# Kernel tuning notes

Hardware: AMD Instinct MI355X
Metric: run time of the kernel (lower is better)

Reference implementation:

```python
import jax, jax.numpy as jnp
from jax import lax
import numpy as np

# Config mirroring init_kwargs
B, N, PD = 4, 16384, 3
PROJ = 64                 # projection_channel
M1, K1, C1 = 2048, 32, 128  # level-1 SA: fps points, neighbors, out channel
M2, K2, C2 = 512, 32, 256   # level-2 SA
DH, DO = 512, 256           # dense hidden / out (dense_channels)


def fps(pts, M):
    """Farthest point sampling. pts: [N,3] -> indices [M] (starts at point 0)."""
    n = pts.shape[0]
    def step(carry, _):
        dmin, last = carry
        d = jnp.sum((pts - pts[last]) ** 2, axis=-1)   # dist to newest center
        dmin = jnp.minimum(dmin, d)
        nxt = jnp.argmax(dmin).astype(jnp.int32)
        return (dmin, nxt), last
    init = (jnp.full((n,), 1e10, pts.dtype), jnp.int32(0))
    _, idxs = lax.scan(step, init, None, length=M)
    return idxs


def sa_level(pts, feats, M, K, Wa, ba, Wb, bb):
    """PointNet++ set abstraction: FPS + kNN (xyz space) + grouped MLP + max."""
    idx = jax.vmap(lambda p: fps(p, M))(pts)                       # [B,M]
    centers = jnp.take_along_axis(pts, idx[:, :, None], axis=1)    # [B,M,3]
    d = jnp.sum((centers[:, :, None, :] - pts[:, None, :, :]) ** 2, -1)  # [B,M,N]
    _, nidx = lax.top_k(-d, K)                                      # [B,M,K]
    gather = jax.vmap(lambda a, i: a[i])
    rel = gather(pts, nidx) - centers[:, :, None, :]                # [B,M,K,3]
    nf = gather(feats, nidx)                                        # [B,M,K,C]
    g = jnp.concatenate([rel, nf], axis=-1)                         # use_xyz=True
    h = jax.nn.relu(g @ Wa + ba)
    h = jax.nn.relu(h @ Wb + bb)
    return centers, jnp.max(h, axis=2)                              # [B,M,Cout]


def setup_inputs() -> dict:
    key = jax.random.key(0)
    ks = jax.random.split(key, 12)
    w = lambda k, shape, s: jax.random.normal(k, shape, jnp.float32) * s
    z = lambda c: jnp.zeros((c,), jnp.float32)
    return {
        "xyz": jax.random.normal(ks[0], (B, N, PD), jnp.float32),
        "Wp": w(ks[1], (PD, PROJ), 0.3), "bp": z(PROJ),
        "W1a": w(ks[2], (PROJ + 3, C1), 0.1), "b1a": z(C1),
        "W1b": w(ks[3], (C1, C1), 0.08), "b1b": z(C1),
        "W2a": w(ks[4], (C1 + 3, C2), 0.08), "b2a": z(C2),
        "W2b": w(ks[5], (C2, C2), 0.06), "b2b": z(C2),
        "Wd1": w(ks[6], (2 * C2, DH), 0.05), "bd1": z(DH),
        "Wd2": w(ks[7], (DH, DO), 0.05), "bd2": z(DO),
    }


def reference(xyz, Wp, bp, W1a, b1a, W1b, b1b, W2a, b2a, W2b, b2b,
              Wd1, bd1, Wd2, bd2):
    feats = xyz @ Wp + bp            # point_proj: [B,N,PROJ]
    pts = xyz[..., :3]
    pts, feats = sa_level(pts, feats, M1, K1, W1a, b1a, W1b, b1b)
    pts, feats = sa_level(pts, feats, M2, K2, W2a, b2a, W2b, b2b)
    # global max + avg pool (adaptive_max/avg_pool1d to 1), concat -> [B,2*C2]
    g = jnp.concatenate([jnp.max(feats, axis=1), jnp.mean(feats, axis=1)], -1)
    h = jax.nn.relu(g @ Wd1 + bd1)   # DenseBlock w/ activation
    return h @ Wd2 + bd2             # last block: no activation (last_activation=False)
```

## Files before the change

kernel.cpp:

```cpp
#include <hip/hip_runtime.h>

#define B_    4
#define N1_   16384
#define M1_   2048
#define M2_   512
#define KNN_  32
#define PROJ_ 64
#define C1_   128
#define C2_   256
#define PROJ_BLKS_ ((B_ * N1_ * PROJ_) / 512)
#define KNN_BLKS_  ((M1_ / 64) * (B_ * 64))

__device__ __forceinline__ float sqdist_exact(float px, float py, float pz,
                                              float cx, float cy, float cz) {
    float dx = __fsub_rn(px, cx);
    float dy = __fsub_rn(py, cy);
    float dz = __fsub_rn(pz, cz);
    return __fadd_rn(__fadd_rn(__fmul_rn(dx, dx), __fmul_rn(dy, dy)), __fmul_rn(dz, dz));
}

typedef float v2f __attribute__((ext_vector_type(2)));

template<int CTRL, int RM>
__device__ __forceinline__ unsigned long long dpp_umax64(unsigned long long pk) {
    unsigned lo = (unsigned)__builtin_amdgcn_update_dpp(
        0, (int)(unsigned)pk, CTRL, RM, 0xf, true);
    unsigned hi = (unsigned)__builtin_amdgcn_update_dpp(
        0, (int)(unsigned)(pk >> 32), CTRL, RM, 0xf, true);
    unsigned long long o = ((unsigned long long)hi << 32) | (unsigned long long)lo;
    return (o > pk) ? o : pk;
}

__device__ __forceinline__ unsigned long long wave_max_key(unsigned long long pk) {
    pk = dpp_umax64<0x111, 0xf>(pk);
    pk = dpp_umax64<0x112, 0xf>(pk);
    pk = dpp_umax64<0x114, 0xf>(pk);
    pk = dpp_umax64<0x118, 0xf>(pk);
    pk = dpp_umax64<0x142, 0xa>(pk);
    pk = dpp_umax64<0x143, 0xc>(pk);
    return pk;
}

__device__ __forceinline__ unsigned reduce8_widx(const unsigned long long* wk,
                                                 int lane) {
    unsigned long long k8 = wk[lane & 7];
    k8 = dpp_umax64<0x111, 0xf>(k8);
    k8 = dpp_umax64<0x112, 0xf>(k8);
    k8 = dpp_umax64<0x114, 0xf>(k8);
    unsigned lo = (unsigned)__builtin_amdgcn_readlane((int)(unsigned)k8, 7);
    return ~lo;
}

__device__ __forceinline__ unsigned reduce2_widx(const unsigned long long* wk,
                                                 int lane) {
    unsigned long long k2 = wk[lane & 1];
    k2 = dpp_umax64<0x111, 0xf>(k2);
    unsigned lo = (unsigned)__builtin_amdgcn_readlane((int)(unsigned)k2, 1);
    return ~lo;
}

template<int N>
__device__ void knn_body512(const float* __restrict__ P,
                            float cx, float cy, float cz,
                            int* __restrict__ out, char* arena) {
    constexpr int K = KNN_;
    constexpr int CAP = 224;
    const int t = threadIdx.x;
    const int lane = t & 63;
    const int w = t >> 6;

    int*      hist = (int*)arena;
    unsigned* eqk  = (unsigned*)(arena + 8192);
    int*      eqi  = (int*)(arena + 8192 + 896);
    int*      wsum = (int*)(arena + 8192 + 1792);
    int*      ctrl = (int*)(arena + 8192 + 1824);

    unsigned prefix = 0; int pbits = 0;
    unsigned Tlo = 0; unsigned long long Thi = 0x100000000ull;
    int L = 0, target = K, Cbin = N;

    for (int round = 0; round < 3; ++round) {
        const int bits  = (round < 2) ? 11 : 10;
        const int nbins = 1 << bits;
        const int shift = 32 - pbits - bits;
        for (int i = t; i < nbins; i += 512) hist[i] = 0;
        __syncthreads();
        for (int j = t; j < N; j += 512) {
            float d = sqdist_exact(P[j * 3], P[j * 3 + 1], P[j * 3 + 2], cx, cy, cz);
            unsigned key = __float_as_uint(d);
            if (key >= Tlo && (unsigned long long)key < Thi)
                atomicAdd(&hist[(key >> shift) & (nbins - 1)], 1);
        }
        __syncthreads();
        const int per = nbins / 512;
        int s = 0;
        for (int i = 0; i < per; ++i) s += hist[t * per + i];
        int cum = s;
        for (int off = 1; off < 64; off <<= 1) {
            int o = __shfl_up(cum, off);
            if (lane >= off) cum += o;
        }
        if (lane == 63) wsum[w] = cum;
        __syncthreads();
        int wpre = 0;
        for (int i = 0; i < w; ++i) wpre += wsum[i];
        cum += wpre;
        const int cumex = cum - s;
        if ((cumex < target) && (cum >= target)) {
            int acc = cumex;
            for (int i = 0; i < per; ++i) {
                int h = hist[t * per + i];
                if (acc + h >= target) { ctrl[2] = t * per + i; ctrl[3] = acc; ctrl[4] = h; break; }
                acc += h;
            }
        }
        __syncthreads();
        const int binsel = ctrl[2];
        const int Ladd   = ctrl[3];
        const int bincnt = ctrl[4];
        L += Ladd;
        target -= Ladd;
        prefix = (prefix << bits) | (unsigned)binsel;
        pbits += bits;
        Tlo = prefix << (32 - pbits);
        Thi = ((unsigned long long)prefix + 1ull) << (32 - pbits);
        Cbin = bincnt;
        __syncthreads();
        if (Cbin <= CAP) break;
    }

    if (t == 0) { ctrl[0] = 0; ctrl[1] = 0; }
    __syncthreads();

    if (Cbin <= CAP) {
        for (int j = t; j < N; j += 512) {
            float d = sqdist_exact(P[j * 3], P[j * 3 + 1], P[j * 3 + 2], cx, cy, cz);
            unsigned key = __float_as_uint(d);
            if (key < Tlo) {
                int p = atomicAdd(&ctrl[0], 1);
                out[p] = j;
            } else if ((unsigned long long)key < Thi) {
                int p = atomicAdd(&ctrl[1], 1);
                eqk[p] = key; eqi[p] = j;
            }
        }
        __syncthreads();
        const int E = ctrl[1];
        for (int e = t; e < E; e += 512) {
            unsigned ke = eqk[e]; int ie = eqi[e];
            int rank = 0;
            for (int f = 0; f < E; ++f) {
                unsigned kf = eqk[f]; int jf = eqi[f];
                rank += (kf < ke || (kf == ke && jf < ie)) ? 1 : 0;
            }
            if (rank < target) out[L + rank] = ie;
        }
    } else {
        if (t < 64) {
            int cnt = 0;
            for (int jb = 0; jb < N; jb += 64) {
                int j = jb + lane;
                float d = sqdist_exact(P[j * 3], P[j * 3 + 1], P[j * 3 + 2], cx, cy, cz);
                unsigned key = __float_as_uint(d);
                if (key < Tlo) {
                    int p = atomicAdd(&ctrl[0], 1);
                    out[p] = j;
                }
                bool eq = (key == Tlo);
                unsigned long long mb = __ballot(eq);
                int below = __popcll(mb & ((1ull << lane) - 1ull));
                if (eq && (cnt + below) < target) out[L + cnt + below] = j;
                cnt += (int)__popcll(mb);
            }
        }
    }
}

__global__ __attribute__((amdgpu_flat_work_group_size(512, 512)))
__attribute__((amdgpu_waves_per_eu(2, 2)))
void mega1_kernel(const float* __restrict__ xyz,
                  const float* __restrict__ Wp, const float* __restrict__ bp,
                  float* __restrict__ feats0, float* __restrict__ centers1,
                  int* __restrict__ nidx1, unsigned* __restrict__ prog) {
#pragma clang fp contract(off)
    __shared__ alignas(16) char arena[24832];
    asm volatile("" ::: "v255");
    const int bid = blockIdx.x;
    const int t = threadIdx.x;

    if (bid >= B_ + PROJ_BLKS_) {
        const int k = bid - (B_ + PROJ_BLKS_);
        const int c = k >> 8;
        const int b = (k >> 6) & 3;
        const int m = c * 64 + (k & 63);
        if (t == 0) {
            while (__hip_atomic_load(&prog[b * 16], __ATOMIC_RELAXED,
                                     __HIP_MEMORY_SCOPE_AGENT) <= (unsigned)c)
                __builtin_amdgcn_s_sleep(16);
        }
        __syncthreads();
        const unsigned* cw = (const unsigned*)(centers1 + ((size_t)b * M1_ + m) * 3);
        float cx = __uint_as_float(__hip_atomic_load(cw + 0, __ATOMIC_RELAXED, __HIP_MEMORY_SCOPE_AGENT));
        float cy = __uint_as_float(__hip_atomic_load(cw + 1, __ATOMIC_RELAXED, __HIP_MEMORY_SCOPE_AGENT));
        float cz = __uint_as_float(__hip_atomic_load(cw + 2, __ATOMIC_RELAXED, __HIP_MEMORY_SCOPE_AGENT));
        knn_body512<N1_>(xyz + (size_t)b * N1_ * 3, cx, cy, cz,
                         nidx1 + ((size_t)b * M1_ + m) * KNN_, arena);
        return;
    }
    if (bid >= B_) {
        int tid = (bid - B_) * 512 + t;
        int cc = tid & (PROJ_ - 1);
        int pn = tid >> 6;
        const float* p = xyz + (size_t)pn * 3;
        float acc = p[0] * Wp[0 * PROJ_ + cc];
        acc = __fmaf_rn(p[1], Wp[1 * PROJ_ + cc], acc);
        acc = __fmaf_rn(p[2], Wp[2 * PROJ_ + cc], acc);
        feats0[tid] = acc + bp[cc];
        return;
    }
    constexpr int NT = 512;
    constexpr int NW = NT / 64;
    constexpr int NP1 = (N1_ / NT) / 2;
    const int b = bid;
    const int w = t >> 6;
    const int lane = t & 63;
    const float* P = xyz + (size_t)b * N1_ * 3;
    float* C1 = centers1 + (size_t)b * M1_ * 3;

    unsigned long long (*wkey)[NW] = (unsigned long long(*)[NW])arena;
    float* cb1 = (float*)(arena + 128);

    v2f px2[NP1], py2[NP1], pz2[NP1];
    float dmin[2 * NP1];
#pragma unroll
    for (int p = 0; p < NP1; ++p) {
        const int j0 = (2 * p) * NT + t;
        const int j1 = j0 + NT;
        px2[p] = (v2f){P[j0 * 3 + 0], P[j1 * 3 + 0]};
        py2[p] = (v2f){P[j0 * 3 + 1], P[j1 * 3 + 1]};
        pz2[p] = (v2f){P[j0 * 3 + 2], P[j1 * 3 + 2]};
        dmin[2 * p] = 1e10f; dmin[2 * p + 1] = 1e10f;
    }
#pragma unroll
    for (int p = 0; p < NP1; ++p)
        asm volatile("" : "+v"(px2[p]), "+v"(py2[p]), "+v"(pz2[p]));

    float cx = P[0], cy = P[1], cz = P[2];

    for (int m = 0; m < M1_; ++m) {
        if (t == 0) {
            cb1[m * 3 + 0] = cx; cb1[m * 3 + 1] = cy; cb1[m * 3 + 2] = cz;
        }
        if ((m & 63) == 63) {
            __syncthreads();
            const int c = m >> 6;
            if (t < 48)
                ((float4*)C1)[c * 48 + t] = ((const float4*)cb1)[c * 48 + t];
            __syncthreads();
            if (t == 0)
                __hip_atomic_store(&prog[b * 16], (unsigned)(c + 1),
                                   __ATOMIC_RELEASE, __HIP_MEMORY_SCOPE_AGENT);
        }
        if (m == M1_ - 1) break;
        const int par = m & 1;
        const v2f c2x = {cx, cx}, c2y = {cy, cy}, c2z = {cz, cz};
        float bv = -1.0f; int bk = 0;
#pragma unroll
        for (int p = 0; p < NP1; ++p) {
            v2f dx = px2[p] - c2x;
            v2f dy = py2[p] - c2y;
            v2f dz = pz2[p] - c2z;
            v2f d2 = (dx * dx + dy * dy) + dz * dz;
            float nd0 = fminf(dmin[2 * p],     d2.x);
            float nd1 = fminf(dmin[2 * p + 1], d2.y);
            dmin[2 * p]     = nd0;
            dmin[2 * p + 1] = nd1;
            bool g0 = nd0 > bv; bv = g0 ? nd0 : bv; bk = g0 ? 2 * p     : bk;
            bool g1 = nd1 > bv; bv = g1 ? nd1 : bv; bk = g1 ? 2 * p + 1 : bk;
        }
        unsigned gi = (unsigned)(bk * NT + t);
        unsigned long long pk =
            ((unsigned long long)__float_as_uint(bv) << 32) | (unsigned)(~gi);
        pk = wave_max_key(pk);
        if (lane == 63) wkey[par][w] = pk;
        __syncthreads();
        const unsigned widx = reduce8_widx(wkey[par], lane);
        const float* cp = P + (size_t)widx * 3;
        cx = cp[0]; cy = cp[1]; cz = cp[2];
    }
}

__device__ __forceinline__ void fps2_body(const float* __restrict__ centers1,
                                          float* __restrict__ centers2,
                                          char* arena) {
#pragma clang fp contract(off)
    constexpr int NT = 128;
    constexpr int NW = 2;
    constexpr int NP = (M1_ / NT) / 2;
    const int b = blockIdx.x;
    const int t = threadIdx.x;
    const int w = t >> 6;
    const int lane = t & 63;
    const float* P = centers1 + (size_t)b * M1_ * 3;
    float* C = centers2 + (size_t)b * M2_ * 3;

    unsigned long long (*wkey)[NW] = (unsigned long long(*)[NW])arena;
    float* cb2 = (float*)(arena + 64);

    v2f px2[NP], py2[NP], pz2[NP];
    float dmin[2 * NP];
#pragma unroll
    for (int p = 0; p < NP; ++p) {
        const int j0 = (2 * p) * NT + t;
        const int j1 = j0 + NT;
        px2[p] = (v2f){P[j0 * 3 + 0], P[j1 * 3 + 0]};
        py2[p] = (v2f){P[j0 * 3 + 1], P[j1 * 3 + 1]};
        pz2[p] = (v2f){P[j0 * 3 + 2], P[j1 * 3 + 2]};
        dmin[2 * p] = 1e10f; dmin[2 * p + 1] = 1e10f;
    }
#pragma unroll
    for (int p = 0; p < NP; ++p)
        asm volatile("" : "+v"(px2[p]), "+v"(py2[p]), "+v"(pz2[p]));

    float cx = P[0], cy = P[1], cz = P[2];

    for (int m = 0; m < M2_; ++m) {
        if (t == 0) {
            cb2[m * 3 + 0] = cx; cb2[m * 3 + 1] = cy; cb2[m * 3 + 2] = cz;
        }
        if (m == M2_ - 1) break;
        const int par = m & 1;
        const v2f c2x = {cx, cx}, c2y = {cy, cy}, c2z = {cz, cz};
        float bv = -1.0f; int bk = 0;
#pragma unroll
        for (int p = 0; p < NP; ++p) {
            v2f dx = px2[p] - c2x;
            v2f dy = py2[p] - c2y;
            v2f dz = pz2[p] - c2z;
            v2f d2 = (dx * dx + dy * dy) + dz * dz;
            float nd0 = fminf(dmin[2 * p],     d2.x);
            float nd1 = fminf(dmin[2 * p + 1], d2.y);
            dmin[2 * p]     = nd0;
            dmin[2 * p + 1] = nd1;
            bool g0 = nd0 > bv; bv = g0 ? nd0 : bv; bk = g0 ? 2 * p     : bk;
            bool g1 = nd1 > bv; bv = g1 ? nd1 : bv; bk = g1 ? 2 * p + 1 : bk;
        }
        unsigned gi = (unsigned)(bk * NT + t);
        unsigned long long pk =
            ((unsigned long long)__float_as_uint(bv) << 32) | (unsigned)(~gi);
        pk = wave_max_key(pk);
        if (lane == 63) wkey[par][w] = pk;
        __syncthreads();
        const unsigned widx = reduce2_widx(wkey[par], lane);
        const float* cp = P + (size_t)widx * 3;
        cx = cp[0]; cy = cp[1]; cz = cp[2];
    }
    __syncthreads();
#pragma unroll 1
    for (int i = t; i < (M2_ * 3) / 4; i += NT)
        ((float4*)C)[i] = ((const float4*)cb2)[i];
}

template<int NPTS, int FD, int CO, int M>
__device__ __forceinline__ void mlp_body(int bm, char* arena,
                 const float* __restrict__ pts, const float* __restrict__ feats,
                 const float* __restrict__ centers, const int* __restrict__ nidx,
                 const float* __restrict__ Wa, const float* __restrict__ ba,
                 const float* __restrict__ Wb, const float* __restrict__ bb,
                 float* __restrict__ outf) {
    constexpr int KN = KNN_;
    constexpr int GS = FD + 4;
    const int b = bm / M;
    const int t = threadIdx.x;
    float (*g)[GS]  = (float(*)[GS])arena;
    float (*h1)[CO] = (float(*)[CO])(arena + sizeof(float) * KN * GS);
    const int* nb = nidx + (size_t)bm * KN;
    const float* cen = centers + (size_t)bm * 3;
    const float cx = cen[0], cy = cen[1], cz = cen[2];
    {
        constexpr int PARTS = CO / KN;
        constexpr int CHUNK = FD / PARTS;
        const int kk = t / PARTS;
        const int q  = t % PARTS;
        const int j  = nb[kk];
        const float* f = feats + ((size_t)b * NPTS + j) * FD + q * CHUNK;
        float* gr = &g[kk][q * CHUNK];
#pragma unroll
        for (int u = 0; u < CHUNK / 4; ++u)
            *(float4*)(gr + 4 * u) = *(const float4*)(f + 4 * u);
        if (q == 0) {
            const float* p = pts + ((size_t)b * NPTS + j) * 3;
            g[kk][FD + 0] = __fsub_rn(p[0], cx);
            g[kk][FD + 1] = __fsub_rn(p[1], cy);
            g[kk][FD + 2] = __fsub_rn(p[2], cz);
            g[kk][FD + 3] = 0.f;
        }
    }
    __syncthreads();
    const int o = t;
    float acc[KN];
#pragma unroll
    for (int k = 0; k < KN; ++k) acc[k] = ba[o];
    for (int s4 = 0; s4 < FD / 4; ++s4) {
        const float w0 = Wa[(4 * s4 + 3) * CO + o];
        const float w1 = Wa[(4 * s4 + 4) * CO + o];
        const float w2 = Wa[(4 * s4 + 5) * CO + o];
        const float w3 = Wa[(4 * s4 + 6) * CO + o];
#pragma unroll
        for (int k = 0; k < KN; ++k) {
            float4 gv = *(const float4*)&g[k][4 * s4];
            acc[k] = __fmaf_rn(gv.x, w0, acc[k]);
            acc[k] = __fmaf_rn(gv.y, w1, acc[k]);
            acc[k] = __fmaf_rn(gv.z, w2, acc[k]);
            acc[k] = __fmaf_rn(gv.w, w3, acc[k]);
        }
    }
    {
        const float w0 = Wa[0 * CO + o];
        const float w1 = Wa[1 * CO + o];
        const float w2 = Wa[2 * CO + o];
#pragma unroll
        for (int k = 0; k < KN; ++k) {
            float4 gv = *(const float4*)&g[k][FD];
            acc[k] = __fmaf_rn(gv.x, w0, acc[k]);
            acc[k] = __fmaf_rn(gv.y, w1, acc[k]);
            acc[k] = __fmaf_rn(gv.z, w2, acc[k]);
        }
    }
#pragma unroll
    for (int k = 0; k < KN; ++k) h1[k][o] = fmaxf(acc[k], 0.f);
    __syncthreads();
#pragma unroll
    for (int k = 0; k < KN; ++k) acc[k] = bb[o];
    for (int s4 = 0; s4 < CO / 4; ++s4) {
        const float w0 = Wb[(4 * s4 + 0) * CO + o];
        const float w1 = Wb[(4 * s4 + 1) * CO + o];
        const float w2 = Wb[(4 * s4 + 2) * CO + o];
        const float w3 = Wb[(4 * s4 + 3) * CO + o];
#pragma unroll
        for (int k = 0; k < KN; ++k) {
            float4 hv = *(const float4*)&h1[k][4 * s4];
            acc[k] = __fmaf_rn(hv.x, w0, acc[k]);
            acc[k] = __fmaf_rn(hv.y, w1, acc[k]);
            acc[k] = __fmaf_rn(hv.z, w2, acc[k]);
            acc[k] = __fmaf_rn(hv.w, w3, acc[k]);
        }
    }
    float mx = 0.f;
#pragma unroll
    for (int k = 0; k < KN; ++k) mx = fmaxf(mx, fmaxf(acc[k], 0.f));
    outf[(size_t)bm * CO + o] = mx;
}

__global__ void __launch_bounds__(C1_)
sa1_kernel(const float* __restrict__ xyz, const float* __restrict__ feats0,
           const float* __restrict__ centers1, const int* __restrict__ nidx1,
           const float* __restrict__ W1a, const float* __restrict__ b1a,
           const float* __restrict__ W1b, const float* __restrict__ b1b,
           float* __restrict__ feats1, float* __restrict__ centers2) {
    constexpr size_t MLP_BYTES =
        sizeof(float) * (KNN_ * (PROJ_ + 4) + KNN_ * C1_);
    __shared__ alignas(16) char arena[MLP_BYTES];
    if (blockIdx.x < B_) {
        fps2_body(centers1, centers2, arena);
        return;
    }
    mlp_body<N1_, PROJ_, C1_, M1_>(blockIdx.x - B_, arena, xyz, feats0,
                                   centers1, nidx1, W1a, b1a, W1b, b1b, feats1);
}

template<int NPTS, int FD, int CO, int M>
__global__ void __launch_bounds__(CO)
group_mlp_kernel(const float* __restrict__ pts, const float* __restrict__ feats,
                 const float* __restrict__ centers, const int* __restrict__ nidx,
                 const float* __restrict__ Wa, const float* __restrict__ ba,
                 const float* __restrict__ Wb, const float* __restrict__ bb,
                 float* __restrict__ outf) {
    constexpr size_t BYTES = sizeof(float) * (KNN_ * (FD + 4) + KNN_ * CO);
    __shared__ alignas(16) char arena[BYTES];
    mlp_body<NPTS, FD, CO, M>(blockIdx.x, arena, pts, feats, centers, nidx,
                              Wa, ba, Wb, bb, outf);
}

template<int N, int M>
__global__ void __launch_bounds__(64)
knn_kernel(const float* __restrict__ pts, const float* __restrict__ centers,
           int* __restrict__ nidx) {
    constexpr int K = KNN_;
    constexpr int CAP = 224;
    const int bm = blockIdx.x;
    const int b = bm / M;
    const int lane = threadIdx.x;
    const float* P = pts + (size_t)b * N * 3;
    const float* c = centers + (size_t)bm * 3;
    const float cx = c[0], cy = c[1], cz = c[2];
    int* out = nidx + (size_t)bm * K;

    __shared__ int hist[2048];
    __shared__ unsigned int eqk[CAP];
    __shared__ int eqi[CAP];
    __shared__ int cnt_less, cnt_eq;

    unsigned int prefix = 0; int pbits = 0;
    unsigned int Tlo = 0; unsigned long long Thi = 0x100000000ull;
    int L = 0, target = K, Cbin = N;

    for (int round = 0; round < 3; ++round) {
        const int bits  = (round < 2) ? 11 : 10;
        const int nbins = 1 << bits;
        const int shift = 32 - pbits - bits;
        for (int i = lane; i < nbins; i += 64) hist[i] = 0;
        __syncthreads();
        for (int j = lane; j < N; j += 64) {
            float d = sqdist_exact(P[j * 3], P[j * 3 + 1], P[j * 3 + 2], cx, cy, cz);
            unsigned int key = __float_as_uint(d);
            if (key >= Tlo && (unsigned long long)key < Thi)
                atomicAdd(&hist[(key >> shift) & (nbins - 1)], 1);
        }
        __syncthreads();
        const int per = nbins / 64;
        int s = 0;
        for (int i = 0; i < per; ++i) s += hist[lane * per + i];
        int cum = s;
        for (int off = 1; off < 64; off <<= 1) {
            int o = __shfl_up(cum, off);
            if (lane >= off) cum += o;
        }
        int cumex = cum - s;
        bool has = (cumex < target) && (cum >= target);
        unsigned long long ball = __ballot(has);
        int src = __ffsll(ball) - 1;
        int binsel = 0, Ladd = 0, bincnt = 0;
        if (lane == src) {
            int acc = cumex;
            for (int i = 0; i < per; ++i) {
                int h = hist[lane * per + i];
                if (acc + h >= target) { binsel = lane * per + i; Ladd = acc; bincnt = h; break; }
                acc += h;
            }
        }
        binsel = __shfl(binsel, src);
        Ladd   = __shfl(Ladd, src);
        bincnt = __shfl(bincnt, src);
        L += Ladd;
        target -= Ladd;
        prefix = (prefix << bits) | (unsigned int)binsel;
        pbits += bits;
        Tlo = prefix << (32 - pbits);
        Thi = ((unsigned long long)prefix + 1ull) << (32 - pbits);
        Cbin = bincnt;
        __syncthreads();
        if (Cbin <= CAP) break;
    }

    if (lane == 0) { cnt_less = 0; cnt_eq = 0; }
    __syncthreads();

    if (Cbin <= CAP) {
        for (int j = lane; j < N; j += 64) {
            float d = sqdist_exact(P[j * 3], P[j * 3 + 1], P[j * 3 + 2], cx, cy, cz);
            unsigned int key = __float_as_uint(d);
            if (key < Tlo) {
                int p = atomicAdd(&cnt_less, 1);
                out[p] = j;
            } else if ((unsigned long long)key < Thi) {
                int p = atomicAdd(&cnt_eq, 1);
                eqk[p] = key; eqi[p] = j;
            }
        }
        __syncthreads();
        const int E = cnt_eq;
        for (int e = lane; e < E; e += 64) {
            unsigned int ke = eqk[e]; int ie = eqi[e];
            int rank = 0;
            for (int f = 0; f < E; ++f) {
                unsigned int kf = eqk[f]; int jf = eqi[f];
                rank += (kf < ke || (kf == ke && jf < ie)) ? 1 : 0;
            }
            if (rank < target) out[L + rank] = ie;
        }
    } else {
        int cnt = 0;
        for (int jb = 0; jb < N; jb += 64) {
            int j = jb + lane;
            float d = sqdist_exact(P[j * 3], P[j * 3 + 1], P[j * 3 + 2], cx, cy, cz);
            unsigned int key = __float_as_uint(d);
            if (key < Tlo) {
                int p = atomicAdd(&cnt_less, 1);
                out[p] = j;
            }
            bool eq = (key == Tlo);
            unsigned long long mb = __ballot(eq);
            int below = __popcll(mb & ((1ull << lane) - 1ull));
            if (eq && (cnt + below) < target) out[L + cnt + below] = j;
            cnt += (int)__popcll(mb);
        }
    }
}

__global__ void __launch_bounds__(256)
head_kernel(const float* __restrict__ feats2,
            const float* __restrict__ Wd1, const float* __restrict__ bd1,
            const float* __restrict__ Wd2, const float* __restrict__ bd2,
            float* __restrict__ outp) {
    const int b = blockIdx.x, t = threadIdx.x;
    __shared__ float gsh[2 * C2_];
    __shared__ float hsh[512];
    const float* F = feats2 + (size_t)b * M2_ * C2_;
    float mx = -1e30f, sm = 0.f;
    for (int r = 0; r < M2_; ++r) {
        float v = F[r * C2_ + t];
        mx = fmaxf(mx, v);
        sm += v;
    }
    gsh[t] = mx;
    gsh[C2_ + t] = sm * (1.0f / (float)M2_);
    __syncthreads();
#pragma unroll
    for (int oo = 0; oo < 2; ++oo) {
        const int o = t + oo * 256;
        float acc = bd1[o];
        for (int i = 0; i < 512; ++i)
            acc = __fmaf_rn(gsh[i], Wd1[i * 512 + o], acc);
        hsh[o] = fmaxf(acc, 0.f);
    }
    __syncthreads();
    float acc = bd2[t];
    for (int i = 0; i < 512; ++i)
        acc = __fmaf_rn(hsh[i], Wd2[i * 256 + t], acc);
    outp[b * 256 + t] = acc;
}

extern "C" void kernel_launch(void* const* d_in, const int* in_sizes, int n_in,
                              void* d_out, int out_size, void* d_ws, size_t ws_size,
                              hipStream_t stream) {
    const float* xyz = (const float*)d_in[0];
    const float* Wp  = (const float*)d_in[1];
    const float* bp  = (const float*)d_in[2];
    const float* W1a = (const float*)d_in[3];
    const float* b1a = (const float*)d_in[4];
    const float* W1b = (const float*)d_in[5];
    const float* b1b = (const float*)d_in[6];
    const float* W2a = (const float*)d_in[7];
    const float* b2a = (const float*)d_in[8];
    const float* W2b = (const float*)d_in[9];
    const float* b2b = (const float*)d_in[10];
    const float* Wd1 = (const float*)d_in[11];
    const float* bd1 = (const float*)d_in[12];
    const float* Wd2 = (const float*)d_in[13];
    const float* bd2 = (const float*)d_in[14];
    float* out = (float*)d_out;

    char* ws = (char*)d_ws;
    size_t off = 0;
    auto alloc = [&](size_t bytes) { void* p = ws + off; off += (bytes + 255) & ~(size_t)255; return p; };
    float* feats0   = (float*)alloc((size_t)B_ * N1_ * PROJ_ * 4);
    float* centers1 = (float*)alloc((size_t)B_ * M1_ * 3 * 4);
    int*   nidx1    = (int*)  alloc((size_t)B_ * M1_ * KNN_ * 4);
    float* feats1   = (float*)alloc((size_t)B_ * M1_ * C1_ * 4);
    float* centers2 = (float*)alloc((size_t)B_ * M2_ * 3 * 4);
    int*   nidx2    = (int*)  alloc((size_t)B_ * M2_ * KNN_ * 4);
    float* feats2   = (float*)alloc((size_t)B_ * M2_ * C2_ * 4);
    unsigned* prog  = (unsigned*)alloc(B_ * 16 * 4);
    (void)in_sizes; (void)n_in; (void)out_size; (void)ws_size;

    hipMemsetAsync(prog, 0, B_ * 16 * 4, stream);

    mega1_kernel<<<dim3(B_ + PROJ_BLKS_ + KNN_BLKS_), dim3(512), 0, stream>>>(
        xyz, Wp, bp, feats0, centers1, nidx1, prog);
    sa1_kernel<<<dim3(B_ + B_ * M1_), dim3(C1_), 0, stream>>>(
        xyz, feats0, centers1, nidx1, W1a, b1a, W1b, b1b, feats1, centers2);
    knn_kernel<M1_, M2_><<<dim3(B_ * M2_), dim3(64), 0, stream>>>(centers1, centers2, nidx2);
    group_mlp_kernel<M1_, C1_, C2_, M2_><<<dim3(B_ * M2_), dim3(C2_), 0, stream>>>(
        centers1, feats1, centers2, nidx2, W2a, b2a, W2b, b2b, feats2);
    head_kernel<<<dim3(B_), dim3(256), 0, stream>>>(feats2, Wd1, bd1, Wd2, bd2, out);
}
```

Measured before the change: 3.858 ms.

## Fuse both SA levels into one persistent megakernel with flag-based dataflow

Merges the level-1 grouped MLP, the level-2 FPS, the level-2 kNN and the level-2 grouped MLP into the single megakernel that already ran projection, FPS1 and kNN1. Stages are ordered by block index and synchronised through per-batch and per-chunk progress counters in global memory. The level-2 kNN moves from a 64-thread kernel to the 512-thread histogram path. The aim is to overlap stages and remove kernel-launch boundaries, at the cost of spin-waiting blocks, a larger shared arena (lower occupancy) and relying on block dispatch order to avoid deadlock.

```diff
diff --git a/kernel.cpp b/kernel.cpp
--- a/kernel.cpp
+++ b/kernel.cpp
@@ -8,8 +8,13 @@
 #define PROJ_ 64
 #define C1_   128
 #define C2_   256
-#define PROJ_BLKS_ ((B_ * N1_ * PROJ_) / 512)
-#define KNN_BLKS_  ((M1_ / 64) * (B_ * 64))
+
+#define PROJ_OFF_   4
+#define KNN1_OFF_   (PROJ_OFF_ + 8192)
+#define MLP1_OFF_   (KNN1_OFF_ + 8192)
+#define KNN2_OFF_   (MLP1_OFF_ + 8192)
+#define MLP2_OFF_   (KNN2_OFF_ + 2048)
+#define TOTAL_BLKS_ (MLP2_OFF_ + 2048)
 
 __device__ __forceinline__ float sqdist_exact(float px, float py, float pz,
                                               float cx, float cy, float cz) {
@@ -18,6 +23,24 @@
     float dz = __fsub_rn(pz, cz);
     return __fadd_rn(__fadd_rn(__fmul_rn(dx, dx), __fmul_rn(dy, dy)), __fmul_rn(dz, dz));
 }
+
+__device__ __forceinline__ float aload(const float* p) {
+    return __uint_as_float(__hip_atomic_load((const unsigned*)p,
+                           __ATOMIC_RELAXED, __HIP_MEMORY_SCOPE_AGENT));
+}
+__device__ __forceinline__ int aiload(const int* p) {
+    return __hip_atomic_load(p, __ATOMIC_RELAXED, __HIP_MEMORY_SCOPE_AGENT);
+}
+__device__ __forceinline__ unsigned auload(const unsigned* p) {
+    return __hip_atomic_load(p, __ATOMIC_RELAXED, __HIP_MEMORY_SCOPE_AGENT);
+}
+
+__device__ __forceinline__ unsigned* f_prog1(unsigned* f, int b) { return f + b * 16; }
+__device__ __forceinline__ unsigned* f_prog2(unsigned* f, int b) { return f + 64 + b * 16; }
+__device__ __forceinline__ unsigned* f_proj (unsigned* f)        { return f + 128; }
+__device__ __forceinline__ unsigned* f_knn1 (unsigned* f, int b, int c) { return f + 192 + (b * 32 + c) * 16; }
+__device__ __forceinline__ unsigned* f_mlp1 (unsigned* f, int b) { return f + 2240 + b * 16; }
+__device__ __forceinline__ unsigned* f_knn2 (unsigned* f, int b, int c) { return f + 2304 + (b * 8 + c) * 16; }
 
 typedef float v2f __attribute__((ext_vector_type(2)));
 
@@ -51,15 +74,7 @@
     return ~lo;
 }
 
-__device__ __forceinline__ unsigned reduce2_widx(const unsigned long long* wk,
-                                                 int lane) {
-    unsigned long long k2 = wk[lane & 1];
-    k2 = dpp_umax64<0x111, 0xf>(k2);
-    unsigned lo = (unsigned)__builtin_amdgcn_readlane((int)(unsigned)k2, 1);
-    return ~lo;
-}
-
-template<int N>
+template<int N, bool AP>
 __device__ void knn_body512(const float* __restrict__ P,
                             float cx, float cy, float cz,
                             int* __restrict__ out, char* arena) {
@@ -86,8 +101,10 @@
         for (int i = t; i < nbins; i += 512) hist[i] = 0;
         __syncthreads();
         for (int j = t; j < N; j += 512) {
-            float d = sqdist_exact(P[j * 3], P[j * 3 + 1], P[j * 3 + 2], cx, cy, cz);
-            unsigned key = __float_as_uint(d);
+            float px = AP ? aload(P + j * 3 + 0) : P[j * 3 + 0];
+            float py = AP ? aload(P + j * 3 + 1) : P[j * 3 + 1];
+            float pz = AP ? aload(P + j * 3 + 2) : P[j * 3 + 2];
+            unsigned key = __float_as_uint(sqdist_exact(px, py, pz, cx, cy, cz));
             if (key >= Tlo && (unsigned long long)key < Thi)
                 atomicAdd(&hist[(key >> shift) & (nbins - 1)], 1);
         }
@@ -134,8 +151,10 @@
 
     if (Cbin <= CAP) {
         for (int j = t; j < N; j += 512) {
-            float d = sqdist_exact(P[j * 3], P[j * 3 + 1], P[j * 3 + 2], cx, cy, cz);
-            unsigned key = __float_as_uint(d);
+            float px = AP ? aload(P + j * 3 + 0) : P[j * 3 + 0];
+            float py = AP ? aload(P + j * 3 + 1) : P[j * 3 + 1];
+            float pz = AP ? aload(P + j * 3 + 2) : P[j * 3 + 2];
+            unsigned key = __float_as_uint(sqdist_exact(px, py, pz, cx, cy, cz));
             if (key < Tlo) {
                 int p = atomicAdd(&ctrl[0], 1);
                 out[p] = j;
@@ -160,8 +179,10 @@
             int cnt = 0;
             for (int jb = 0; jb < N; jb += 64) {
                 int j = jb + lane;
-                float d = sqdist_exact(P[j * 3], P[j * 3 + 1], P[j * 3 + 2], cx, cy, cz);
-                unsigned key = __float_as_uint(d);
+                float px = AP ? aload(P + j * 3 + 0) : P[j * 3 + 0];
+                float py = AP ? aload(P + j * 3 + 1) : P[j * 3 + 1];
+                float pz = AP ? aload(P + j * 3 + 2) : P[j * 3 + 2];
+                unsigned key = __float_as_uint(sqdist_exact(px, py, pz, cx, cy, cz));
                 if (key < Tlo) {
                     int p = atomicAdd(&ctrl[0], 1);
                     out[p] = j;
@@ -176,39 +197,284 @@
     }
 }
 
+__device__ void mega_mlp1(int b, int m, char* arena,
+                          const float* __restrict__ xyz,
+                          const float* __restrict__ feats0,
+                          const float* __restrict__ centers1,
+                          const int* __restrict__ nidx1,
+                          const float* __restrict__ Wa, const float* __restrict__ ba,
+                          const float* __restrict__ Wb, const float* __restrict__ bb,
+                          float* __restrict__ feats1) {
+    constexpr int KN = KNN_, FD = PROJ_, CO = C1_, GS = FD + 4;
+    const int t = threadIdx.x;
+    const size_t bm = (size_t)b * M1_ + m;
+    float (*g)[GS]  = (float(*)[GS])arena;
+    float (*h1)[CO] = (float(*)[CO])(arena + sizeof(float) * KN * GS);
+    const int* nb = nidx1 + bm * KN;
+    if (t < CO) {
+        const float* cen = centers1 + bm * 3;
+        const float cx = aload(cen + 0), cy = aload(cen + 1), cz = aload(cen + 2);
+        constexpr int PARTS = CO / KN;
+        constexpr int CHUNK = FD / PARTS;
+        const int kk = t / PARTS;
+        const int q  = t % PARTS;
+        const int j  = aiload(&nb[kk]);
+        const float* f = feats0 + ((size_t)b * N1_ + j) * FD + q * CHUNK;
+        float* gr = &g[kk][q * CHUNK];
+#pragma unroll
+        for (int u = 0; u < CHUNK; ++u) gr[u] = aload(f + u);
+        if (q == 0) {
+            const float* p = xyz + ((size_t)b * N1_ + j) * 3;
+            g[kk][FD + 0] = __fsub_rn(p[0], cx);
+            g[kk][FD + 1] = __fsub_rn(p[1], cy);
+            g[kk][FD + 2] = __fsub_rn(p[2], cz);
+            g[kk][FD + 3] = 0.f;
+        }
+    }
+    __syncthreads();
+    if (t < CO) {
+        const int o = t;
+        float acc[KN];
+#pragma unroll
+        for (int k = 0; k < KN; ++k) acc[k] = ba[o];
+        for (int s4 = 0; s4 < FD / 4; ++s4) {
+            const float w0 = Wa[(4 * s4 + 3) * CO + o];
+            const float w1 = Wa[(4 * s4 + 4) * CO + o];
+            const float w2 = Wa[(4 * s4 + 5) * CO + o];
+            const float w3 = Wa[(4 * s4 + 6) * CO + o];
+#pragma unroll
+            for (int k = 0; k < KN; ++k) {
+                float4 gv = *(const float4*)&g[k][4 * s4];
+                acc[k] = __fmaf_rn(gv.x, w0, acc[k]);
+                acc[k] = __fmaf_rn(gv.y, w1, acc[k]);
+                acc[k] = __fmaf_rn(gv.z, w2, acc[k]);
+                acc[k] = __fmaf_rn(gv.w, w3, acc[k]);
+            }
+        }
+        {
+            const float w0 = Wa[0 * CO + o];
+            const float w1 = Wa[1 * CO + o];
+            const float w2 = Wa[2 * CO + o];
+#pragma unroll
+            for (int k = 0; k < KN; ++k) {
+                float4 gv = *(const float4*)&g[k][FD];
+                acc[k] = __fmaf_rn(gv.x, w0, acc[k]);
+                acc[k] = __fmaf_rn(gv.y, w1, acc[k]);
+                acc[k] = __fmaf_rn(gv.z, w2, acc[k]);
+            }
+        }
+#pragma unroll
+        for (int k = 0; k < KN; ++k) h1[k][o] = fmaxf(acc[k], 0.f);
+    }
+    __syncthreads();
+    if (t < CO) {
+        const int o = t;
+        float acc[KN];
+#pragma unroll
+        for (int k = 0; k < KN; ++k) acc[k] = bb[o];
+        for (int s4 = 0; s4 < CO / 4; ++s4) {
+            const float w0 = Wb[(4 * s4 + 0) * CO + o];
+            const float w1 = Wb[(4 * s4 + 1) * CO + o];
+            const float w2 = Wb[(4 * s4 + 2) * CO + o];
+            const float w3 = Wb[(4 * s4 + 3) * CO + o];
+#pragma unroll
+            for (int k = 0; k < KN; ++k) {
+                float4 hv = *(const float4*)&h1[k][4 * s4];
+                acc[k] = __fmaf_rn(hv.x, w0, acc[k]);
+                acc[k] = __fmaf_rn(hv.y, w1, acc[k]);
+                acc[k] = __fmaf_rn(hv.z, w2, acc[k]);
+                acc[k] = __fmaf_rn(hv.w, w3, acc[k]);
+            }
+        }
+        float mx = 0.f;
+#pragma unroll
+        for (int k = 0; k < KN; ++k) mx = fmaxf(mx, fmaxf(acc[k], 0.f));
+        feats1[bm * CO + o] = mx;
+    }
+}
+
+__device__ void mega_mlp2(int b, int m, char* arena,
+                          const float* __restrict__ centers1,
+                          const float* __restrict__ feats1,
+                          const float* __restrict__ centers2,
+                          const int* __restrict__ nidx2,
+                          const float* __restrict__ Wa, const float* __restrict__ ba,
+                          const float* __restrict__ Wb, const float* __restrict__ bb,
+                          float* __restrict__ feats2) {
+    constexpr int KN = KNN_, FD = C1_, CO = C2_, GS = FD + 4;
+    const int t = threadIdx.x;
+    const size_t bm = (size_t)b * M2_ + m;
+    float (*g)[GS]  = (float(*)[GS])arena;
+    float (*h1)[CO] = (float(*)[CO])(arena + sizeof(float) * KN * GS);
+    const int* nb = nidx2 + bm * KN;
+    if (t < CO) {
+        const float* cen = centers2 + bm * 3;
+        const float cx = aload(cen + 0), cy = aload(cen + 1), cz = aload(cen + 2);
+        constexpr int PARTS = CO / KN;
+        constexpr int CHUNK = FD / PARTS;
+        const int kk = t / PARTS;
+        const int q  = t % PARTS;
+        const int j  = aiload(&nb[kk]);
+        const float* f = feats1 + ((size_t)b * M1_ + j) * FD + q * CHUNK;
+        float* gr = &g[kk][q * CHUNK];
+#pragma unroll
+        for (int u = 0; u < CHUNK; ++u) gr[u] = aload(f + u);
+        if (q == 0) {
+            const float* p = centers1 + ((size_t)b * M1_ + j) * 3;
+            g[kk][FD + 0] = __fsub_rn(aload(p + 0), cx);
+            g[kk][FD + 1] = __fsub_rn(aload(p + 1), cy);
+            g[kk][FD + 2] = __fsub_rn(aload(p + 2), cz);
+            g[kk][FD + 3] = 0.f;
+        }
+    }
+    __syncthreads();
+    if (t < CO) {
+        const int o = t;
+        float acc[KN];
+#pragma unroll
+        for (int k = 0; k < KN; ++k) acc[k] = ba[o];
+        for (int s4 = 0; s4 < FD / 4; ++s4) {
+            const float w0 = Wa[(4 * s4 + 3) * CO + o];
+            const float w1 = Wa[(4 * s4 + 4) * CO + o];
+            const float w2 = Wa[(4 * s4 + 5) * CO + o];
+            const float w3 = Wa[(4 * s4 + 6) * CO + o];
+#pragma unroll
+            for (int k = 0; k < KN; ++k) {
+                float4 gv = *(const float4*)&g[k][4 * s4];
+                acc[k] = __fmaf_rn(gv.x, w0, acc[k]);
+                acc[k] = __fmaf_rn(gv.y, w1, acc[k]);
+                acc[k] = __fmaf_rn(gv.z, w2, acc[k]);
+                acc[k] = __fmaf_rn(gv.w, w3, acc[k]);
+            }
+        }
+        {
+            const float w0 = Wa[0 * CO + o];
+            const float w1 = Wa[1 * CO + o];
+            const float w2 = Wa[2 * CO + o];
+#pragma unroll
+            for (int k = 0; k < KN; ++k) {
+                float4 gv = *(const float4*)&g[k][FD];
+                acc[k] = __fmaf_rn(gv.x, w0, acc[k]);
+                acc[k] = __fmaf_rn(gv.y, w1, acc[k]);
+                acc[k] = __fmaf_rn(gv.z, w2, acc[k]);
+            }
+        }
+#pragma unroll
+        for (int k = 0; k < KN; ++k) h1[k][o] = fmaxf(acc[k], 0.f);
+    }
+    __syncthreads();
+    if (t < CO) {
+        const int o = t;
+        float acc[KN];
+#pragma unroll
+        for (int k = 0; k < KN; ++k) acc[k] = bb[o];
+        for (int s4 = 0; s4 < CO / 4; ++s4) {
+            const float w0 = Wb[(4 * s4 + 0) * CO + o];
+            const float w1 = Wb[(4 * s4 + 1) * CO + o];
+            const float w2 = Wb[(4 * s4 + 2) * CO + o];
+            const float w3 = Wb[(4 * s4 + 3) * CO + o];
+#pragma unroll
+            for (int k = 0; k < KN; ++k) {
+                float4 hv = *(const float4*)&h1[k][4 * s4];
+                acc[k] = __fmaf_rn(hv.x, w0, acc[k]);
+                acc[k] = __fmaf_rn(hv.y, w1, acc[k]);
+                acc[k] = __fmaf_rn(hv.z, w2, acc[k]);
+                acc[k] = __fmaf_rn(hv.w, w3, acc[k]);
+            }
+        }
+        float mx = 0.f;
+#pragma unroll
+        for (int k = 0; k < KN; ++k) mx = fmaxf(mx, fmaxf(acc[k], 0.f));
+        feats2[bm * CO + o] = mx;
+    }
+}
+
 __global__ __attribute__((amdgpu_flat_work_group_size(512, 512)))
 __attribute__((amdgpu_waves_per_eu(2, 2)))
-void mega1_kernel(const float* __restrict__ xyz,
-                  const float* __restrict__ Wp, const float* __restrict__ bp,
-                  float* __restrict__ feats0, float* __restrict__ centers1,
-                  int* __restrict__ nidx1, unsigned* __restrict__ prog) {
+void mega_kernel(const float* __restrict__ xyz,
+                 const float* __restrict__ Wp, const float* __restrict__ bp,
+                 const float* __restrict__ W1a, const float* __restrict__ b1a,
+                 const float* __restrict__ W1b, const float* __restrict__ b1b,
+                 const float* __restrict__ W2a, const float* __restrict__ b2a,
+                 const float* __restrict__ W2b, const float* __restrict__ b2b,
+                 float* __restrict__ feats0, float* __restrict__ centers1,
+                 int* __restrict__ nidx1, float* __restrict__ feats1,
+                 float* __restrict__ centers2, int* __restrict__ nidx2,
+                 float* __restrict__ feats2, unsigned* __restrict__ flags) {
 #pragma clang fp contract(off)
-    __shared__ alignas(16) char arena[24832];
+    __shared__ alignas(16) char arena[49664];
     asm volatile("" ::: "v255");
     const int bid = blockIdx.x;
     const int t = threadIdx.x;
 
-    if (bid >= B_ + PROJ_BLKS_) {
-        const int k = bid - (B_ + PROJ_BLKS_);
-        const int c = k >> 8;
-        const int b = (k >> 6) & 3;
-        const int m = c * 64 + (k & 63);
+    if (bid >= MLP2_OFF_) {
+        const int k = bid - MLP2_OFF_;
+        const int c = k >> 8, b = (k >> 6) & 3, m = c * 64 + (k & 63);
         if (t == 0) {
-            while (__hip_atomic_load(&prog[b * 16], __ATOMIC_RELAXED,
-                                     __HIP_MEMORY_SCOPE_AGENT) <= (unsigned)c)
+            while (auload(f_knn2(flags, b, c)) < 64u ||
+                   auload(f_mlp1(flags, b)) < (unsigned)M1_)
                 __builtin_amdgcn_s_sleep(16);
         }
         __syncthreads();
-        const unsigned* cw = (const unsigned*)(centers1 + ((size_t)b * M1_ + m) * 3);
-        float cx = __uint_as_float(__hip_atomic_load(cw + 0, __ATOMIC_RELAXED, __HIP_MEMORY_SCOPE_AGENT));
-        float cy = __uint_as_float(__hip_atomic_load(cw + 1, __ATOMIC_RELAXED, __HIP_MEMORY_SCOPE_AGENT));
-        float cz = __uint_as_float(__hip_atomic_load(cw + 2, __ATOMIC_RELAXED, __HIP_MEMORY_SCOPE_AGENT));
-        knn_body512<N1_>(xyz + (size_t)b * N1_ * 3, cx, cy, cz,
-                         nidx1 + ((size_t)b * M1_ + m) * KNN_, arena);
+        mega_mlp2(b, m, arena, centers1, feats1, centers2, nidx2,
+                  W2a, b2a, W2b, b2b, feats2);
         return;
     }
-    if (bid >= B_) {
-        int tid = (bid - B_) * 512 + t;
+    if (bid >= KNN2_OFF_) {
+        const int k = bid - KNN2_OFF_;
+        const int c = k >> 8, b = (k >> 6) & 3, m = c * 64 + (k & 63);
+        if (t == 0) {
+            while (auload(f_prog2(flags, b)) <= (unsigned)c)
+                __builtin_amdgcn_s_sleep(16);
+        }
+        __syncthreads();
+        const float* cw = centers2 + ((size_t)b * M2_ + m) * 3;
+        float cx = aload(cw + 0), cy = aload(cw + 1), cz = aload(cw + 2);
+        knn_body512<M1_, true>(centers1 + (size_t)b * M1_ * 3, cx, cy, cz,
+                               nidx2 + ((size_t)b * M2_ + m) * KNN_, arena);
+        __syncthreads();
+        if (t == 0)
+            __hip_atomic_fetch_add(f_knn2(flags, b, c), 1u,
+                                   __ATOMIC_RELEASE, __HIP_MEMORY_SCOPE_AGENT);
+        return;
+    }
+    if (bid >= MLP1_OFF_) {
+        const int k = bid - MLP1_OFF_;
+        const int c = k >> 8, b = (k >> 6) & 3, m = c * 64 + (k & 63);
+        if (t == 0) {
+            while (auload(f_knn1(flags, b, c)) < 64u ||
+                   auload(f_proj(flags)) < 8192u)
+                __builtin_amdgcn_s_sleep(16);
+        }
+        __syncthreads();
+        mega_mlp1(b, m, arena, xyz, feats0, centers1, nidx1,
+                  W1a, b1a, W1b, b1b, feats1);
+        __syncthreads();
+        if (t == 0)
+            __hip_atomic_fetch_add(f_mlp1(flags, b), 1u,
+                                   __ATOMIC_RELEASE, __HIP_MEMORY_SCOPE_AGENT);
+        return;
+    }
+    if (bid >= KNN1_OFF_) {
+        const int k = bid - KNN1_OFF_;
+        const int c = k >> 8, b = (k >> 6) & 3, m = c * 64 + (k & 63);
+        if (t == 0) {
+            while (auload(f_prog1(flags, b)) <= (unsigned)c)
+                __builtin_amdgcn_s_sleep(16);
+        }
+        __syncthreads();
+        const float* cw = centers1 + ((size_t)b * M1_ + m) * 3;
+        float cx = aload(cw + 0), cy = aload(cw + 1), cz = aload(cw + 2);
+        knn_body512<N1_, false>(xyz + (size_t)b * N1_ * 3, cx, cy, cz,
+                                nidx1 + ((size_t)b * M1_ + m) * KNN_, arena);
+        __syncthreads();
+        if (t == 0)
+            __hip_atomic_fetch_add(f_knn1(flags, b, c), 1u,
+                                   __ATOMIC_RELEASE, __HIP_MEMORY_SCOPE_AGENT);
+        return;
+    }
+    if (bid >= PROJ_OFF_) {
+        int tid = (bid - PROJ_OFF_) * 512 + t;
         int cc = tid & (PROJ_ - 1);
         int pn = tid >> 6;
         const float* p = xyz + (size_t)pn * 3;
@@ -216,384 +482,147 @@
         acc = __fmaf_rn(p[1], Wp[1 * PROJ_ + cc], acc);
         acc = __fmaf_rn(p[2], Wp[2 * PROJ_ + cc], acc);
         feats0[tid] = acc + bp[cc];
+        __syncthreads();
+        if (t == 0)
+            __hip_atomic_fetch_add(f_proj(flags), 1u,
+                                   __ATOMIC_RELEASE, __HIP_MEMORY_SCOPE_AGENT);
         return;
     }
     constexpr int NT = 512;
     constexpr int NW = NT / 64;
-    constexpr int NP1 = (N1_ / NT) / 2;
     const int b = bid;
     const int w = t >> 6;
     const int lane = t & 63;
     const float* P = xyz + (size_t)b * N1_ * 3;
     float* C1 = centers1 + (size_t)b * M1_ * 3;
+    float* C2 = centers2 + (size_t)b * M2_ * 3;
 
     unsigned long long (*wkey)[NW] = (unsigned long long(*)[NW])arena;
     float* cb1 = (float*)(arena + 128);
-
-    v2f px2[NP1], py2[NP1], pz2[NP1];
-    float dmin[2 * NP1];
-#pragma unroll
-    for (int p = 0; p < NP1; ++p) {
-        const int j0 = (2 * p) * NT + t;
-        const int j1 = j0 + NT;
-        px2[p] = (v2f){P[j0 * 3 + 0], P[j1 * 3 + 0]};
-        py2[p] = (v2f){P[j0 * 3 + 1], P[j1 * 3 + 1]};
-        pz2[p] = (v2f){P[j0 * 3 + 2], P[j1 * 3 + 2]};
-        dmin[2 * p] = 1e10f; dmin[2 * p + 1] = 1e10f;
-    }
-#pragma unroll
-    for (int p = 0; p < NP1; ++p)
-        asm volatile("" : "+v"(px2[p]), "+v"(py2[p]), "+v"(pz2[p]));
-
-    float cx = P[0], cy = P[1], cz = P[2];
-
-    for (int m = 0; m < M1_; ++m) {
-        if (t == 0) {
-            cb1[m * 3 + 0] = cx; cb1[m * 3 + 1] = cy; cb1[m * 3 + 2] = cz;
-        }
-        if ((m & 63) == 63) {
+    float* cb2 = (float*)(arena + 24704);
+
+    {
+        constexpr int NP1 = (N1_ / NT) / 2;
+        v2f px2[NP1], py2[NP1], pz2[NP1];
+        float dmin[2 * NP1];
+#pragma unroll
+        for (int p = 0; p < NP1; ++p) {
+            const int j0 = (2 * p) * NT + t;
+            const int j1 = j0 + NT;
+            px2[p] = (v2f){P[j0 * 3 + 0], P[j1 * 3 + 0]};
+            py2[p] = (v2f){P[j0 * 3 + 1], P[j1 * 3 + 1]};
+            pz2[p] = (v2f){P[j0 * 3 + 2], P[j1 * 3 + 2]};
+            dmin[2 * p] = 1e10f; dmin[2 * p + 1] = 1e10f;
+        }
+#pragma unroll
+        for (int p = 0; p < NP1; ++p)
+            asm volatile("" : "+v"(px2[p]), "+v"(py2[p]), "+v"(pz2[p]));
+
+        float cx = P[0], cy = P[1], cz = P[2];
+
+        for (int m = 0; m < M1_; ++m) {
+            if (t == 0) {
+                cb1[m * 3 + 0] = cx; cb1[m * 3 + 1] = cy; cb1[m * 3 + 2] = cz;
+            }
+            if ((m & 63) == 63) {
+                __syncthreads();
+                const int c = m >> 6;
+                if (t < 48)
+                    ((float4*)C1)[c * 48 + t] = ((const float4*)cb1)[c * 48 + t];
+                __syncthreads();
+                if (t == 0)
+                    __hip_atomic_store(f_prog1(flags, b), (unsigned)(c + 1),
+                                       __ATOMIC_RELEASE, __HIP_MEMORY_SCOPE_AGENT);
+            }
+            if (m == M1_ - 1) break;
+            const int par = m & 1;
+            const v2f c2x = {cx, cx}, c2y = {cy, cy}, c2z = {cz, cz};
+            float bv = -1.0f; int bk = 0;
+#pragma unroll
+            for (int p = 0; p < NP1; ++p) {
+                v2f dx = px2[p] - c2x;
+                v2f dy = py2[p] - c2y;
+                v2f dz = pz2[p] - c2z;
+                v2f d2 = (dx * dx + dy * dy) + dz * dz;
+                float nd0 = fminf(dmin[2 * p],     d2.x);
+                float nd1 = fminf(dmin[2 * p + 1], d2.y);
+                dmin[2 * p]     = nd0;
+                dmin[2 * p + 1] = nd1;
+                bool g0 = nd0 > bv; bv = g0 ? nd0 : bv; bk = g0 ? 2 * p     : bk;
+                bool g1 = nd1 > bv; bv = g1 ? nd1 : bv; bk = g1 ? 2 * p + 1 : bk;
+            }
+            unsigned gi = (unsigned)(bk * NT + t);
+            unsigned long long pk =
+                ((unsigned long long)__float_as_uint(bv) << 32) | (unsigned)(~gi);
+            pk = wave_max_key(pk);
+            if (lane == 63) wkey[par][w] = pk;
             __syncthreads();
-            const int c = m >> 6;
-            if (t < 48)
-                ((float4*)C1)[c * 48 + t] = ((const float4*)cb1)[c * 48 + t];
+            const unsigned widx = reduce8_widx(wkey[par], lane);
+            const float* cp = P + (size_t)widx * 3;
+            cx = cp[0]; cy = cp[1]; cz = cp[2];
+        }
+    }
+    __syncthreads();
+    {
+        constexpr int NP = (M1_ / NT) / 2;
+        v2f px2[NP], py2[NP], pz2[NP];
+        float dmin[2 * NP];
+#pragma unroll
+        for (int p = 0; p < NP; ++p) {
+            const int j0 = (2 * p) * NT + t;
+            const int j1 = j0 + NT;
+            px2[p] = (v2f){cb1[j0 * 3 + 0], cb1[j1 * 3 + 0]};
+            py2[p] = (v2f){cb1[j0 * 3 + 1], cb1[j1 * 3 + 1]};
+            pz2[p] = (v2f){cb1[j0 * 3 + 2], cb1[j1 * 3 + 2]};
+            dmin[2 * p] = 1e10f; dmin[2 * p + 1] = 1e10f;
+        }
+#pragma unroll
+        for (int p = 0; p < NP; ++p)
+            asm volatile("" : "+v"(px2[p]), "+v"(py2[p]), "+v"(pz2[p]));
+
+        float cx = cb1[0], cy = cb1[1], cz = cb1[2];
+
+        for (int m = 0; m < M2_; ++m) {
+            if (t == 0) {
+                cb2[m * 3 + 0] = cx; cb2[m * 3 + 1] = cy; cb2[m * 3 + 2] = cz;
+            }
+            if ((m & 63) == 63) {
+                __syncthreads();
+                const int c = m >> 6;
+                if (t < 48)
+                    ((float4*)C2)[c * 48 + t] = ((const float4*)cb2)[c * 48 + t];
+                __syncthreads();
+                if (t == 0)
+                    __hip_atomic_store(f_prog2(flags, b), (unsigned)(c + 1),
+                                       __ATOMIC_RELEASE, __HIP_MEMORY_SCOPE_AGENT);
+            }
+            if (m == M2_ - 1) break;
+            const int par = m & 1;
+            const v2f c2x = {cx, cx}, c2y = {cy, cy}, c2z = {cz, cz};
+            float bv = -1.0f; int bk = 0;
+#pragma unroll
+            for (int p = 0; p < NP; ++p) {
+                v2f dx = px2[p] - c2x;
+                v2f dy = py2[p] - c2y;
+                v2f dz = pz2[p] - c2z;
+                v2f d2 = (dx * dx + dy * dy) + dz * dz;
+                float nd0 = fminf(dmin[2 * p],     d2.x);
+                float nd1 = fminf(dmin[2 * p + 1], d2.y);
+                dmin[2 * p]     = nd0;
+                dmin[2 * p + 1] = nd1;
+                bool g0 = nd0 > bv; bv = g0 ? nd0 : bv; bk = g0 ? 2 * p     : bk;
+                bool g1 = nd1 > bv; bv = g1 ? nd1 : bv; bk = g1 ? 2 * p + 1 : bk;
+            }
+            unsigned gi = (unsigned)(bk * NT + t);
+            unsigned long long pk =
+                ((unsigned long long)__float_as_uint(bv) << 32) | (unsigned)(~gi);
+            pk = wave_max_key(pk);
+            if (lane == 63) wkey[par][w] = pk;
             __syncthreads();
-            if (t == 0)
-                __hip_atomic_store(&prog[b * 16], (unsigned)(c + 1),
-                                   __ATOMIC_RELEASE, __HIP_MEMORY_SCOPE_AGENT);
-        }
-        if (m == M1_ - 1) break;
-        const int par = m & 1;
-        const v2f c2x = {cx, cx}, c2y = {cy, cy}, c2z = {cz, cz};
-        float bv = -1.0f; int bk = 0;
-#pragma unroll
-        for (int p = 0; p < NP1; ++p) {
-            v2f dx = px2[p] - c2x;
-            v2f dy = py2[p] - c2y;
-            v2f dz = pz2[p] - c2z;
-            v2f d2 = (dx * dx + dy * dy) + dz * dz;
-            float nd0 = fminf(dmin[2 * p],     d2.x);
-            float nd1 = fminf(dmin[2 * p + 1], d2.y);
-            dmin[2 * p]     = nd0;
-            dmin[2 * p + 1] = nd1;
-            bool g0 = nd0 > bv; bv = g0 ? nd0 : bv; bk = g0 ? 2 * p     : bk;
-            bool g1 = nd1 > bv; bv = g1 ? nd1 : bv; bk = g1 ? 2 * p + 1 : bk;
-        }
-        unsigned gi = (unsigned)(bk * NT + t);
-        unsigned long long pk =
-            ((unsigned long long)__float_as_uint(bv) << 32) | (unsigned)(~gi);
-        pk = wave_max_key(pk);
-        if (lane == 63) wkey[par][w] = pk;
-        __syncthreads();
-        const unsigned widx = reduce8_widx(wkey[par], lane);
-        const float* cp = P + (size_t)widx * 3;
-        cx = cp[0]; cy = cp[1]; cz = cp[2];
-    }
-}
-
-__device__ __forceinline__ void fps2_body(const float* __restrict__ centers1,
-                                          float* __restrict__ centers2,
-                                          char* arena) {
-#pragma clang fp contract(off)
-    constexpr int NT = 128;
-    constexpr int NW = 2;
-    constexpr int NP = (M1_ / NT) / 2;
-    const int b = blockIdx.x;
-    const int t = threadIdx.x;
-    const int w = t >> 6;
-    const int lane = t & 63;
-    const float* P = centers1 + (size_t)b * M1_ * 3;
-    float* C = centers2 + (size_t)b * M2_ * 3;
-
-    unsigned long long (*wkey)[NW] = (unsigned long long(*)[NW])arena;
-    float* cb2 = (float*)(arena + 64);
-
-    v2f px2[NP], py2[NP], pz2[NP];
-    float dmin[2 * NP];
-#pragma unroll
-    for (int p = 0; p < NP; ++p) {
-        const int j0 = (2 * p) * NT + t;
-        const int j1 = j0 + NT;
-        px2[p] = (v2f){P[j0 * 3 + 0], P[j1 * 3 + 0]};
-        py2[p] = (v2f){P[j0 * 3 + 1], P[j1 * 3 + 1]};
-        pz2[p] = (v2f){P[j0 * 3 + 2], P[j1 * 3 + 2]};
-        dmin[2 * p] = 1e10f; dmin[2 * p + 1] = 1e10f;
-    }
-#pragma unroll
-    for (int p = 0; p < NP; ++p)
-        asm volatile("" : "+v"(px2[p]), "+v"(py2[p]), "+v"(pz2[p]));
-
-    float cx = P[0], cy = P[1], cz = P[2];
-
-    for (int m = 0; m < M2_; ++m) {
-        if (t == 0) {
-            cb2[m * 3 + 0] = cx; cb2[m * 3 + 1] = cy; cb2[m * 3 + 2] = cz;
-        }
-        if (m == M2_ - 1) break;
-        const int par = m & 1;
-        const v2f c2x = {cx, cx}, c2y = {cy, cy}, c2z = {cz, cz};
-        float bv = -1.0f; int bk = 0;
-#pragma unroll
-        for (int p = 0; p < NP; ++p) {
-            v2f dx = px2[p] - c2x;
-            v2f dy = py2[p] - c2y;
-            v2f dz = pz2[p] - c2z;
-            v2f d2 = (dx * dx + dy * dy) + dz * dz;
-            float nd0 = fminf(dmin[2 * p],     d2.x);
-            float nd1 = fminf(dmin[2 * p + 1], d2.y);
-            dmin[2 * p]     = nd0;
-            dmin[2 * p + 1] = nd1;
-            bool g0 = nd0 > bv; bv = g0 ? nd0 : bv; bk = g0 ? 2 * p     : bk;
-            bool g1 = nd1 > bv; bv = g1 ? nd1 : bv; bk = g1 ? 2 * p + 1 : bk;
-        }
-        unsigned gi = (unsigned)(bk * NT + t);
-        unsigned long long pk =
-            ((unsigned long long)__float_as_uint(bv) << 32) | (unsigned)(~gi);
-        pk = wave_max_key(pk);
-        if (lane == 63) wkey[par][w] = pk;
-        __syncthreads();
-        const unsigned widx = reduce2_widx(wkey[par], lane);
-        const float* cp = P + (size_t)widx * 3;
-        cx = cp[0]; cy = cp[1]; cz = cp[2];
-    }
-    __syncthreads();
-#pragma unroll 1
-    for (int i = t; i < (M2_ * 3) / 4; i += NT)
-        ((float4*)C)[i] = ((const float4*)cb2)[i];
-}
-
-template<int NPTS, int FD, int CO, int M>
-__device__ __forceinline__ void mlp_body(int bm, char* arena,
-                 const float* __restrict__ pts, const float* __restrict__ feats,
-                 const float* __restrict__ centers, const int* __restrict__ nidx,
-                 const float* __restrict__ Wa, const float* __restrict__ ba,
-                 const float* __restrict__ Wb, const float* __restrict__ bb,
-                 float* __restrict__ outf) {
-    constexpr int KN = KNN_;
-    constexpr int GS = FD + 4;
-    const int b = bm / M;
-    const int t = threadIdx.x;
-    float (*g)[GS]  = (float(*)[GS])arena;
-    float (*h1)[CO] = (float(*)[CO])(arena + sizeof(float) * KN * GS);
-    const int* nb = nidx + (size_t)bm * KN;
-    const float* cen = centers + (size_t)bm * 3;
-    const float cx = cen[0], cy = cen[1], cz = cen[2];
-    {
-        constexpr int PARTS = CO / KN;
-        constexpr int CHUNK = FD / PARTS;
-        const int kk = t / PARTS;
-        const int q  = t % PARTS;
-        const int j  = nb[kk];
-        const float* f = feats + ((size_t)b * NPTS + j) * FD + q * CHUNK;
-        float* gr = &g[kk][q * CHUNK];
-#pragma unroll
-        for (int u = 0; u < CHUNK / 4; ++u)
-            *(float4*)(gr + 4 * u) = *(const float4*)(f + 4 * u);
-        if (q == 0) {
-            const float* p = pts + ((size_t)b * NPTS + j) * 3;
-            g[kk][FD + 0] = __fsub_rn(p[0], cx);
-            g[kk][FD + 1] = __fsub_rn(p[1], cy);
-            g[kk][FD + 2] = __fsub_rn(p[2], cz);
-            g[kk][FD + 3] = 0.f;
-        }
-    }
-    __syncthreads();
-    const int o = t;
-    float acc[KN];
-#pragma unroll
-    for (int k = 0; k < KN; ++k) acc[k] = ba[o];
-    for (int s4 = 0; s4 < FD / 4; ++s4) {
-        const float w0 = Wa[(4 * s4 + 3) * CO + o];
-        const float w1 = Wa[(4 * s4 + 4) * CO + o];
-        const float w2 = Wa[(4 * s4 + 5) * CO + o];
-        const float w3 = Wa[(4 * s4 + 6) * CO + o];
-#pragma unroll
-        for (int k = 0; k < KN; ++k) {
-            float4 gv = *(const float4*)&g[k][4 * s4];
-            acc[k] = __fmaf_rn(gv.x, w0, acc[k]);
-            acc[k] = __fmaf_rn(gv.y, w1, acc[k]);
-            acc[k] = __fmaf_rn(gv.z, w2, acc[k]);
-            acc[k] = __fmaf_rn(gv.w, w3, acc[k]);
-        }
-    }
-    {
-        const float w0 = Wa[0 * CO + o];
-        const float w1 = Wa[1 * CO + o];
-        const float w2 = Wa[2 * CO + o];
-#pragma unroll
-        for (int k = 0; k < KN; ++k) {
-            float4 gv = *(const float4*)&g[k][FD];
-            acc[k] = __fmaf_rn(gv.x, w0, acc[k]);
-            acc[k] = __fmaf_rn(gv.y, w1, acc[k]);
-            acc[k] = __fmaf_rn(gv.z, w2, acc[k]);
-        }
-    }
-#pragma unroll
-    for (int k = 0; k < KN; ++k) h1[k][o] = fmaxf(acc[k], 0.f);
-    __syncthreads();
-#pragma unroll
-    for (int k = 0; k < KN; ++k) acc[k] = bb[o];
-    for (int s4 = 0; s4 < CO / 4; ++s4) {
-        const float w0 = Wb[(4 * s4 + 0) * CO + o];
-        const float w1 = Wb[(4 * s4 + 1) * CO + o];
-        const float w2 = Wb[(4 * s4 + 2) * CO + o];
-        const float w3 = Wb[(4 * s4 + 3) * CO + o];
-#pragma unroll
-        for (int k = 0; k < KN; ++k) {
-            float4 hv = *(const float4*)&h1[k][4 * s4];
-            acc[k] = __fmaf_rn(hv.x, w0, acc[k]);
-            acc[k] = __fmaf_rn(hv.y, w1, acc[k]);
-            acc[k] = __fmaf_rn(hv.z, w2, acc[k]);
-            acc[k] = __fmaf_rn(hv.w, w3, acc[k]);
-        }
-    }
-    float mx = 0.f;
-#pragma unroll
-    for (int k = 0; k < KN; ++k) mx = fmaxf(mx, fmaxf(acc[k], 0.f));
-    outf[(size_t)bm * CO + o] = mx;
-}
-
-__global__ void __launch_bounds__(C1_)
-sa1_kernel(const float* __restrict__ xyz, const float* __restrict__ feats0,
-           const float* __restrict__ centers1, const int* __restrict__ nidx1,
-           const float* __restrict__ W1a, const float* __restrict__ b1a,
-           const float* __restrict__ W1b, const float* __restrict__ b1b,
-           float* __restrict__ feats1, float* __restrict__ centers2) {
-    constexpr size_t MLP_BYTES =
-        sizeof(float) * (KNN_ * (PROJ_ + 4) + KNN_ * C1_);
-    __shared__ alignas(16) char arena[MLP_BYTES];
-    if (blockIdx.x < B_) {
-        fps2_body(centers1, centers2, arena);
-        return;
-    }
-    mlp_body<N1_, PROJ_, C1_, M1_>(blockIdx.x - B_, arena, xyz, feats0,
-                                   centers1, nidx1, W1a, b1a, W1b, b1b, feats1);
-}
-
-template<int NPTS, int FD, int CO, int M>
-__global__ void __launch_bounds__(CO)
-group_mlp_kernel(const float* __restrict__ pts, const float* __restrict__ feats,
-                 const float* __restrict__ centers, const int* __restrict__ nidx,
-                 const float* __restrict__ Wa, const float* __restrict__ ba,
-                 const float* __restrict__ Wb, const float* __restrict__ bb,
-                 float* __restrict__ outf) {
-    constexpr size_t BYTES = sizeof(float) * (KNN_ * (FD + 4) + KNN_ * CO);
-    __shared__ alignas(16) char arena[BYTES];
-    mlp_body<NPTS, FD, CO, M>(blockIdx.x, arena, pts, feats, centers, nidx,
-                              Wa, ba, Wb, bb, outf);
-}
-
-template<int N, int M>
-__global__ void __launch_bounds__(64)
-knn_kernel(const float* __restrict__ pts, const float* __restrict__ centers,
-           int* __restrict__ nidx) {
-    constexpr int K = KNN_;
-    constexpr int CAP = 224;
-    const int bm = blockIdx.x;
-    const int b = bm / M;
-    const int lane = threadIdx.x;
-    const float* P = pts + (size_t)b * N * 3;
-    const float* c = centers + (size_t)bm * 3;
-    const float cx = c[0], cy = c[1], cz = c[2];
-    int* out = nidx + (size_t)bm * K;
-
-    __shared__ int hist[2048];
-    __shared__ unsigned int eqk[CAP];
-    __shared__ int eqi[CAP];
-    __shared__ int cnt_less, cnt_eq;
-
-    unsigned int prefix = 0; int pbits = 0;
-    unsigned int Tlo = 0; unsigned long long Thi = 0x100000000ull;
-    int L = 0, target = K, Cbin = N;
-
-    for (int round = 0; round < 3; ++round) {
-        const int bits  = (round < 2) ? 11 : 10;
-        const int nbins = 1 << bits;
-        const int shift = 32 - pbits - bits;
-        for (int i = lane; i < nbins; i += 64) hist[i] = 0;
-        __syncthreads();
-        for (int j = lane; j < N; j += 64) {
-            float d = sqdist_exact(P[j * 3], P[j * 3 + 1], P[j * 3 + 2], cx, cy, cz);
-            unsigned int key = __float_as_uint(d);
-            if (key >= Tlo && (unsigned long long)key < Thi)
-                atomicAdd(&hist[(key >> shift) & (nbins - 1)], 1);
-        }
-        __syncthreads();
-        const int per = nbins / 64;
-        int s = 0;
-        for (int i = 0; i < per; ++i) s += hist[lane * per + i];
-        int cum = s;
-        for (int off = 1; off < 64; off <<= 1) {
-            int o = __shfl_up(cum, off);
-            if (lane >= off) cum += o;
-        }
-        int cumex = cum - s;
-        bool has = (cumex < target) && (cum >= target);
-        unsigned long long ball = __ballot(has);
-        int src = __ffsll(ball) - 1;
-        int binsel = 0, Ladd = 0, bincnt = 0;
-        if (lane == src) {
-            int acc = cumex;
-            for (int i = 0; i < per; ++i) {
-                int h = hist[lane * per + i];
-                if (acc + h >= target) { binsel = lane * per + i; Ladd = acc; bincnt = h; break; }
-                acc += h;
-            }
-        }
-        binsel = __shfl(binsel, src);
-        Ladd   = __shfl(Ladd, src);
-        bincnt = __shfl(bincnt, src);
-        L += Ladd;
-        target -= Ladd;
-        prefix = (prefix << bits) | (unsigned int)binsel;
-        pbits += bits;
-        Tlo = prefix << (32 - pbits);
-        Thi = ((unsigned long long)prefix + 1ull) << (32 - pbits);
-        Cbin = bincnt;
-        __syncthreads();
-        if (Cbin <= CAP) break;
-    }
-
-    if (lane == 0) { cnt_less = 0; cnt_eq = 0; }
-    __syncthreads();
-
-    if (Cbin <= CAP) {
-        for (int j = lane; j < N; j += 64) {
-            float d = sqdist_exact(P[j * 3], P[j * 3 + 1], P[j * 3 + 2], cx, cy, cz);
-            unsigned int key = __float_as_uint(d);
-            if (key < Tlo) {
-                int p = atomicAdd(&cnt_less, 1);
-                out[p] = j;
-            } else if ((unsigned long long)key < Thi) {
-                int p = atomicAdd(&cnt_eq, 1);
-                eqk[p] = key; eqi[p] = j;
-            }
-        }
-        __syncthreads();
-        const int E = cnt_eq;
-        for (int e = lane; e < E; e += 64) {
-            unsigned int ke = eqk[e]; int ie = eqi[e];
-            int rank = 0;
-            for (int f = 0; f < E; ++f) {
-                unsigned int kf = eqk[f]; int jf = eqi[f];
-                rank += (kf < ke || (kf == ke && jf < ie)) ? 1 : 0;
-            }
-            if (rank < target) out[L + rank] = ie;
-        }
-    } else {
-        int cnt = 0;
-        for (int jb = 0; jb < N; jb += 64) {
-            int j = jb + lane;
-            float d = sqdist_exact(P[j * 3], P[j * 3 + 1], P[j * 3 + 2], cx, cy, cz);
-            unsigned int key = __float_as_uint(d);
-            if (key < Tlo) {
-                int p = atomicAdd(&cnt_less, 1);
-                out[p] = j;
-            }
-            bool eq = (key == Tlo);
-            unsigned long long mb = __ballot(eq);
-            int below = __popcll(mb & ((1ull << lane) - 1ull));
-            if (eq && (cnt + below) < target) out[L + cnt + below] = j;
-            cnt += (int)__popcll(mb);
+            const unsigned widx = reduce8_widx(wkey[par], lane);
+            cx = cb1[widx * 3 + 0];
+            cy = cb1[widx * 3 + 1];
+            cz = cb1[widx * 3 + 2];
         }
     }
 }
@@ -661,17 +690,13 @@
     float* centers2 = (float*)alloc((size_t)B_ * M2_ * 3 * 4);
     int*   nidx2    = (int*)  alloc((size_t)B_ * M2_ * KNN_ * 4);
     float* feats2   = (float*)alloc((size_t)B_ * M2_ * C2_ * 4);
-    unsigned* prog  = (unsigned*)alloc(B_ * 16 * 4);
+    unsigned* flags = (unsigned*)alloc(16384);
     (void)in_sizes; (void)n_in; (void)out_size; (void)ws_size;
 
-    hipMemsetAsync(prog, 0, B_ * 16 * 4, stream);
-
-    mega1_kernel<<<dim3(B_ + PROJ_BLKS_ + KNN_BLKS_), dim3(512), 0, stream>>>(
-        xyz, Wp, bp, feats0, centers1, nidx1, prog);
-    sa1_kernel<<<dim3(B_ + B_ * M1_), dim3(C1_), 0, stream>>>(
-        xyz, feats0, centers1, nidx1, W1a, b1a, W1b, b1b, feats1, centers2);
-    knn_kernel<M1_, M2_><<<dim3(B_ * M2_), dim3(64), 0, stream>>>(centers1, centers2, nidx2);
-    group_mlp_kernel<M1_, C1_, C2_, M2_><<<dim3(B_ * M2_), dim3(C2_), 0, stream>>>(
-        centers1, feats1, centers2, nidx2, W2a, b2a, W2b, b2b, feats2);
+    hipMemsetAsync(flags, 0, 16384, stream);
+
+    mega_kernel<<<dim3(TOTAL_BLKS_), dim3(512), 0, stream>>>(
+        xyz, Wp, bp, W1a, b1a, W1b, b1b, W2a, b2a, W2b, b2b,
+        feats0, centers1, nidx1, feats1, centers2, nidx2, feats2, flags);
     head_kernel<<<dim3(B_), dim3(256), 0, stream>>>(feats2, Wd1, bd1, Wd2, bd2, out);
 }
```

New measurement: 4.460 ms. 1.16x slower.
